# Kernel optimization log

Measured on AMD Instinct MI355X. Metric: run time of the kernel, lower is better.

## Reference

```python
import jax, jax.numpy as jnp
import numpy as np

NEG = -1.0e9  # masked_fill value from the original module

def setup_inputs() -> dict:
    key = jax.random.key(0)
    kq, kk, kv, km = jax.random.split(key, 4)
    B, H, S, D = 4, 16, 2048, 64
    Q = jax.random.normal(kq, (B, H, S, D), dtype=jnp.float32)
    K = jax.random.normal(kk, (B, H, S, D), dtype=jnp.float32)
    V = jax.random.normal(kv, (B, H, S, D), dtype=jnp.float32)
    # boolean mask, True = masked out (broadcast over batch and heads)
    mask = jax.random.randint(km, (1, 1, S, S), 0, 2).astype(jnp.bool_)
    return {"Q": Q, "K": K, "V": V, "mask": mask}

def reference(Q, K, V, mask):
    d_k = K.shape[-1]
    scale = 1.0 / jnp.sqrt(jnp.asarray(d_k, dtype=Q.dtype))
    # [B,H,S,S] attention scores
    scores = jnp.einsum("bhqd,bhkd->bhqk", Q, K) * scale
    scores = jnp.where(mask, jnp.asarray(NEG, dtype=scores.dtype), scores)
    weights = jax.nn.softmax(scores, axis=-1)
    # dropout is identity in eval mode (self.training == False)
    return jnp.einsum("bhqk,bhkd->bhqd", weights, V)
```

## Files before the change

### kernel.cpp

```cpp
#include <hip/hip_runtime.h>
#include <stdint.h>

#define SQ 2048
#define DH 64
#define NTILES (SQ / 64)

typedef __attribute__((ext_vector_type(8))) short bf16x8;
typedef __attribute__((ext_vector_type(4))) short bf16x4;
typedef __attribute__((ext_vector_type(4))) float f32x4;

static __device__ __forceinline__ unsigned short f2bf_rne(float x) {
  union { float f; uint32_t u; } v; v.f = x;
  uint32_t u = v.u;
  return (unsigned short)((u + 0x7FFFu + ((u >> 16) & 1u)) >> 16);
}

static __device__ __forceinline__ uint32_t pack_hi(float a, float b) {
  uint32_t au = __float_as_uint(a), bu = __float_as_uint(b);
#if __has_builtin(__builtin_amdgcn_perm)
  return __builtin_amdgcn_perm(bu, au, 0x07060302u);
#else
  return (bu & 0xFFFF0000u) | (au >> 16);
#endif
}

static __device__ __forceinline__ float fast_exp2(float x) {
#if __has_builtin(__builtin_amdgcn_exp2f)
  return __builtin_amdgcn_exp2f(x);
#else
  return exp2f(x);
#endif
}

#if __has_builtin(__builtin_amdgcn_mfma_f32_16x16x16_bf16)
#define MFMA_PV(a, b, c) __builtin_amdgcn_mfma_f32_16x16x16_bf16((a), (b), (c), 0, 0, 0)
#else
#define MFMA_PV(a, b, c) __builtin_amdgcn_mfma_f32_16x16x16bf16_1k((a), (b), (c), 0, 0, 0)
#endif

__global__ void pack_mask_kernel(const int* __restrict__ mask,
                                 unsigned long long* __restrict__ bits) {
  const int lane = threadIdx.x & 63;
  const int gw = (blockIdx.x * blockDim.x + threadIdx.x) >> 6;
  const int nw = (gridDim.x * blockDim.x) >> 6;
  for (int w = gw; w < SQ * SQ / 64; w += nw) {
    int v = mask[(size_t)w * 64 + lane];
    unsigned long long b = __ballot(v != 0);
    if (lane == 0) bits[(size_t)(w & 31) * SQ + (w >> 5)] = b;
  }
}

__global__ __launch_bounds__(512, 4) void attn_kernel(
    const float* __restrict__ Qg, const float* __restrict__ Kg,
    const float* __restrict__ Vg, const unsigned long long* __restrict__ mbits,
    const int* __restrict__ mraw, float* __restrict__ Og) {
  __shared__ __align__(16) unsigned short Klds[2][64][72];
  __shared__ __align__(16) uint32_t Vtlds[2][64][36];

  const int id = blockIdx.x;
  const int bh = id & 63;
  const int qblk = id >> 6;
  const int t = threadIdx.x;
  const int wave = t >> 6;
  const int lane = t & 63;
  const int col = lane & 15;
  const int quad = lane >> 4;

  const float* Qb = Qg + (size_t)bh * SQ * DH;
  const float* Kb = Kg + (size_t)bh * SQ * DH;
  const float* Vb = Vg + (size_t)bh * SQ * DH;
  float* Ob = Og + (size_t)bh * SQ * DH;

  const int q0 = qblk * 256 + wave * 32;

  const int skk = t >> 3;
  const int sd8 = (t & 7) * 8;
  const int skp = t >> 4;
  const int sd4 = (t & 15) * 4;

  const float QSCALE = 0.18033688011112042f;
  bf16x8 qf[2][2];
#pragma unroll
  for (int s = 0; s < 2; ++s) {
    int q = q0 + s * 16 + col;
#pragma unroll
    for (int j = 0; j < 2; ++j) {
      const float4* p = (const float4*)(Qb + (size_t)q * DH + j * 32 + quad * 8);
      float4 a = p[0], b = p[1];
      bf16x8 f;
      f[0] = (short)f2bf_rne(a.x * QSCALE); f[1] = (short)f2bf_rne(a.y * QSCALE);
      f[2] = (short)f2bf_rne(a.z * QSCALE); f[3] = (short)f2bf_rne(a.w * QSCALE);
      f[4] = (short)f2bf_rne(b.x * QSCALE); f[5] = (short)f2bf_rne(b.y * QSCALE);
      f[6] = (short)f2bf_rne(b.z * QSCALE); f[7] = (short)f2bf_rne(b.w * QSCALE);
      qf[s][j] = f;
    }
  }

  f32x4 acc[2][4];
  f32x4 accl[2];
#pragma unroll
  for (int s = 0; s < 2; ++s) {
#pragma unroll
    for (int dt = 0; dt < 4; ++dt)
#pragma unroll
      for (int r = 0; r < 4; ++r) acc[s][dt][r] = 0.0f;
#pragma unroll
    for (int r = 0; r < 4; ++r) accl[s][r] = 0.0f;
  }
  bf16x4 vones;
  vones[0] = (short)0x3F80; vones[1] = (short)0x3F80;
  vones[2] = (short)0x3F80; vones[3] = (short)0x3F80;
  const f32x4 fz = {0.0f, 0.0f, 0.0f, 0.0f};

  auto load_mask = [&](int ti, unsigned long long m[2]) {
    if (mbits) {
#pragma unroll
      for (int s = 0; s < 2; ++s)
        m[s] = mbits[(size_t)ti * SQ + (q0 + s * 16 + col)];
    } else {
#pragma unroll
      for (int s = 0; s < 2; ++s) {
        int q = q0 + s * 16 + col;
        unsigned long long mm = 0;
#pragma unroll
        for (int j = 0; j < 4; ++j) {
          int4 mi = *(const int4*)(mraw + (size_t)q * SQ + ti * 64 + j * 16 + quad * 4);
          unsigned long long nib = (unsigned long long)((mi.x != 0) | ((mi.y != 0) << 1) |
                                                        ((mi.z != 0) << 2) | ((mi.w != 0) << 3));
          mm |= nib << (j * 16 + quad * 4);
        }
        m[s] = mm;
      }
    }
  };

  {
    const float4* kp = (const float4*)(Kb + (size_t)skk * DH + sd8);
    float4 k0 = kp[0], k1 = kp[1];
    const float* va = Vb + (size_t)(skp * 2) * DH + sd4;
    float4 v0 = *(const float4*)va, v1 = *(const float4*)(va + DH);
    uint4 kw;
    kw.x = pack_hi(k0.x, k0.y); kw.y = pack_hi(k0.z, k0.w);
    kw.z = pack_hi(k1.x, k1.y); kw.w = pack_hi(k1.z, k1.w);
    *(uint4*)&Klds[0][skk][sd8] = kw;
    Vtlds[0][sd4 + 0][skp] = pack_hi(v0.x, v1.x);
    Vtlds[0][sd4 + 1][skp] = pack_hi(v0.y, v1.y);
    Vtlds[0][sd4 + 2][skp] = pack_hi(v0.z, v1.z);
    Vtlds[0][sd4 + 3][skp] = pack_hi(v0.w, v1.w);
  }
  unsigned long long mcur[2];
  load_mask(0, mcur);

  for (int tile = 0; tile < NTILES; ++tile) {
    __syncthreads();
    const int cb = tile & 1, nb = cb ^ 1;
    const int tn = (tile + 1 < NTILES) ? tile + 1 : tile;

    const int kkn = tn * 64;
    const float4* kp = (const float4*)(Kb + (size_t)(kkn + skk) * DH + sd8);
    float4 k0 = kp[0], k1 = kp[1];
    const float* va = Vb + (size_t)(kkn + skp * 2) * DH + sd4;
    float4 v0 = *(const float4*)va;
    float4 v1 = *(const float4*)(va + DH);
    unsigned long long mnxt[2];
    load_mask(tn, mnxt);

    uint32_t pfw[2][4][2];
#pragma unroll
    for (int kt = 0; kt < 4; ++kt) {
      const bf16x8 kf0 = *(const bf16x8*)&Klds[cb][kt * 16 + col][quad * 8];
      const bf16x8 kf1 = *(const bf16x8*)&Klds[cb][kt * 16 + col][32 + quad * 8];
#pragma unroll
      for (int s = 0; s < 2; ++s) {
        f32x4 st = __builtin_amdgcn_mfma_f32_16x16x32_bf16(kf0, qf[s][0], fz, 0, 0, 0);
        st = __builtin_amdgcn_mfma_f32_16x16x32_bf16(kf1, qf[s][1], st, 0, 0, 0);
        uint32_t nib = (uint32_t)(mcur[s] >> (kt * 16 + quad * 4)) & 0xFu;
        float p[4];
#pragma unroll
        for (int r = 0; r < 4; ++r)
          p[r] = fast_exp2(((nib >> r) & 1u) ? -1.0e9f : st[r]);
        pfw[s][kt][0] = pack_hi(p[0], p[1]);
        pfw[s][kt][1] = pack_hi(p[2], p[3]);
      }
    }

    {
      uint4 kw;
      kw.x = pack_hi(k0.x, k0.y); kw.y = pack_hi(k0.z, k0.w);
      kw.z = pack_hi(k1.x, k1.y); kw.w = pack_hi(k1.z, k1.w);
      *(uint4*)&Klds[nb][skk][sd8] = kw;
      Vtlds[nb][sd4 + 0][skp] = pack_hi(v0.x, v1.x);
      Vtlds[nb][sd4 + 1][skp] = pack_hi(v0.y, v1.y);
      Vtlds[nb][sd4 + 2][skp] = pack_hi(v0.z, v1.z);
      Vtlds[nb][sd4 + 3][skp] = pack_hi(v0.w, v1.w);
    }
    mcur[0] = mnxt[0]; mcur[1] = mnxt[1];

#pragma unroll
    for (int kt = 0; kt < 4; ++kt) {
      union { uint32_t u[2]; bf16x4 v; } p0, p1;
      p0.u[0] = pfw[0][kt][0]; p0.u[1] = pfw[0][kt][1];
      p1.u[0] = pfw[1][kt][0]; p1.u[1] = pfw[1][kt][1];
      accl[0] = MFMA_PV(vones, p0.v, accl[0]);
      accl[1] = MFMA_PV(vones, p1.v, accl[1]);
#pragma unroll
      for (int dt = 0; dt < 4; ++dt) {
        union { uint2 u2; bf16x4 v; } cv;
        cv.u2 = *(const uint2*)&Vtlds[cb][dt * 16 + col][kt * 8 + quad * 2];
        acc[0][dt] = MFMA_PV(cv.v, p0.v, acc[0][dt]);
        acc[1][dt] = MFMA_PV(cv.v, p1.v, acc[1][dt]);
      }
    }
  }

#pragma unroll
  for (int s = 0; s < 2; ++s) {
    float inv = 1.0f / accl[s][0];
    int q = q0 + s * 16 + col;
    float* orow = Ob + (size_t)q * DH;
#pragma unroll
    for (int dt = 0; dt < 4; ++dt) {
      float4 o;
      o.x = acc[s][dt][0] * inv;
      o.y = acc[s][dt][1] * inv;
      o.z = acc[s][dt][2] * inv;
      o.w = acc[s][dt][3] * inv;
      *(float4*)(orow + dt * 16 + quad * 4) = o;
    }
  }
}

extern "C" void kernel_launch(void* const* d_in, const int* in_sizes, int n_in,
                              void* d_out, int out_size, void* d_ws, size_t ws_size,
                              hipStream_t stream) {
  const float* Q = (const float*)d_in[0];
  const float* K = (const float*)d_in[1];
  const float* V = (const float*)d_in[2];
  const int* mask = (const int*)d_in[3];
  float* out = (float*)d_out;

  unsigned long long* bits = nullptr;
  const size_t need = (size_t)SQ * SQ / 8;
  if (ws_size >= need) {
    bits = (unsigned long long*)d_ws;
    pack_mask_kernel<<<1024, 256, 0, stream>>>(mask, bits);
  }
  attn_kernel<<<512, 512, 0, stream>>>(Q, K, V, bits, mask, out);
}
```

Before: 249.6 us.

## Pre-pack K/V to swizzled bf16 and mask to lane bitmasks before attention

New measurement: 242.8 us. 1.03x faster.

```diff
diff --git a/kernel.cpp b/kernel.cpp
--- a/kernel.cpp
+++ b/kernel.cpp
@@ -3,7 +3,6 @@
 
 #define SQ 2048
 #define DH 64
-#define NTILES (SQ / 64)
 
 typedef __attribute__((ext_vector_type(8))) short bf16x8;
 typedef __attribute__((ext_vector_type(4))) short bf16x4;
@@ -37,6 +36,77 @@
 #else
 #define MFMA_PV(a, b, c) __builtin_amdgcn_mfma_f32_16x16x16bf16_1k((a), (b), (c), 0, 0, 0)
 #endif
+
+
+__global__ __launch_bounds__(256) void pack_KV(const float* __restrict__ K,
+                                               const float* __restrict__ V,
+                                               uint4* __restrict__ pk,
+                                               uint2* __restrict__ pv) {
+  __shared__ uint32_t Vw[64][33];
+  const int bt = blockIdx.x;
+  const int t = threadIdx.x;
+  {
+    const float* src = K + (size_t)bt * 64 * DH;
+    uint4* dst = pk + (size_t)bt * 512;
+#pragma unroll
+    for (int j = 0; j < 2; ++j) {
+      int i = t + j * 256;
+      int kk = i >> 3, cp = i & 7;
+      int c = cp ^ (kk & 7);
+      const float4* s4 = (const float4*)(src + (size_t)kk * DH + c * 8);
+      float4 a = s4[0], b = s4[1];
+      uint4 w;
+      w.x = pack_hi(a.x, a.y); w.y = pack_hi(a.z, a.w);
+      w.z = pack_hi(b.x, b.y); w.w = pack_hi(b.z, b.w);
+      dst[i] = w;
+    }
+  }
+  {
+    const float* src = V + (size_t)bt * 64 * DH;
+#pragma unroll
+    for (int half = 0; half < 2; ++half) {
+      int kp = (t >> 4) + half * 16;
+      int d4 = (t & 15) * 4;
+      float4 a = *(const float4*)(src + (size_t)(2 * kp) * DH + d4);
+      float4 b = *(const float4*)(src + (size_t)(2 * kp + 1) * DH + d4);
+      Vw[d4 + 0][kp] = pack_hi(a.x, b.x);
+      Vw[d4 + 1][kp] = pack_hi(a.y, b.y);
+      Vw[d4 + 2][kp] = pack_hi(a.z, b.z);
+      Vw[d4 + 3][kp] = pack_hi(a.w, b.w);
+    }
+    __syncthreads();
+    uint2* dst = pv + (size_t)bt * 1024;
+#pragma unroll
+    for (int j = 0; j < 4; ++j) {
+      int o = t + j * 256;
+      int d = o >> 4, up = o & 15;
+      int u = up ^ (d & 15);
+      uint2 w;
+      w.x = Vw[d][2 * u]; w.y = Vw[d][2 * u + 1];
+      dst[o] = w;
+    }
+  }
+}
+
+__global__ __launch_bounds__(256) void pack_M(const int* __restrict__ mask,
+                                              uint2* __restrict__ pm) {
+  __shared__ uint2 Lm[16][17];
+  const int qb = blockIdx.x >> 5, gb = blockIdx.x & 31;
+  const int t = threadIdx.x;
+  {
+    int qq = t >> 4, gg = t & 15;
+    int4 m = *(const int4*)(mask + (size_t)(qb * 16 + qq) * SQ + (gb * 16 + gg) * 4);
+    uint2 w;
+    w.x = (m.x ? 0u : 0xFFFFu) | (m.y ? 0u : 0xFFFF0000u);
+    w.y = (m.z ? 0u : 0xFFFFu) | (m.w ? 0u : 0xFFFF0000u);
+    Lm[gg][qq] = w;
+  }
+  __syncthreads();
+  {
+    int gg = t >> 4, qq = t & 15;
+    pm[(size_t)(gb * 16 + gg) * 2048 + qb * 16 + qq] = Lm[gg][qq];
+  }
+}
 
 __global__ void pack_mask_kernel(const int* __restrict__ mask,
                                  unsigned long long* __restrict__ bits) {
@@ -50,33 +120,23 @@
   }
 }
 
-__global__ __launch_bounds__(512, 4) void attn_kernel(
-    const float* __restrict__ Qg, const float* __restrict__ Kg,
-    const float* __restrict__ Vg, const unsigned long long* __restrict__ mbits,
-    const int* __restrict__ mraw, float* __restrict__ Og) {
-  __shared__ __align__(16) unsigned short Klds[2][64][72];
-  __shared__ __align__(16) uint32_t Vtlds[2][64][36];
+__global__ __launch_bounds__(256, 4) void attn2(
+    const uint4* __restrict__ pk, const uint4* __restrict__ pv,
+    const uint2* __restrict__ pm, const float* __restrict__ Qg,
+    float* __restrict__ Og) {
+  __shared__ __align__(16) uint8_t smem[32768];
 
   const int id = blockIdx.x;
   const int bh = id & 63;
   const int qblk = id >> 6;
   const int t = threadIdx.x;
-  const int wave = t >> 6;
-  const int lane = t & 63;
-  const int col = lane & 15;
-  const int quad = lane >> 4;
+  const int wave = t >> 6, lane = t & 63, col = lane & 15, quad = lane >> 4;
 
   const float* Qb = Qg + (size_t)bh * SQ * DH;
-  const float* Kb = Kg + (size_t)bh * SQ * DH;
-  const float* Vb = Vg + (size_t)bh * SQ * DH;
   float* Ob = Og + (size_t)bh * SQ * DH;
-
-  const int q0 = qblk * 256 + wave * 32;
-
-  const int skk = t >> 3;
-  const int sd8 = (t & 7) * 8;
-  const int skp = t >> 4;
-  const int sd4 = (t & 15) * 4;
+  const uint4* pkb = pk + (size_t)bh * 32 * 512;
+  const uint4* pvb = pv + (size_t)bh * 32 * 512;
+  const int q0 = qblk * 128 + wave * 32;
 
   const float QSCALE = 0.18033688011112042f;
   bf16x8 qf[2][2];
@@ -96,6 +156,16 @@
     }
   }
 
+  const unsigned ka0 = col * 128 + ((quad ^ (col & 7)) * 16);
+  const unsigned ka1 = col * 128 + (((4 + quad) ^ (col & 7)) * 16);
+  unsigned va[4];
+#pragma unroll
+  for (int kt = 0; kt < 4; ++kt)
+    va[kt] = 16384u + col * 128 + (((kt * 4 + quad) ^ col) * 8);
+  const unsigned stK = t * 16;
+  const unsigned stV = 16384u + t * 16;
+  const size_t mqB = (size_t)(quad * 2048 + q0 + col) * 8;
+
   f32x4 acc[2][4];
   f32x4 accl[2];
 #pragma unroll
@@ -112,6 +182,134 @@
   vones[2] = (short)0x3F80; vones[3] = (short)0x3F80;
   const f32x4 fz = {0.0f, 0.0f, 0.0f, 0.0f};
 
+  {
+    uint4 k0 = pkb[t], k1 = pkb[t + 256];
+    uint4 v0 = pvb[t], v1 = pvb[t + 256];
+    *(uint4*)(smem + stK) = k0; *(uint4*)(smem + stK + 4096) = k1;
+    *(uint4*)(smem + stV) = v0; *(uint4*)(smem + stV + 4096) = v1;
+  }
+  unsigned buf = 0;
+
+  for (int tile = 0; tile < 32; ++tile) {
+    __syncthreads();
+    const int tn = (tile < 31) ? tile + 1 : 31;
+
+    const uint4* pkt = pkb + (size_t)tn * 512;
+    const uint4* pvt = pvb + (size_t)tn * 512;
+    uint4 k0 = pkt[t], k1 = pkt[t + 256];
+    uint4 v0 = pvt[t], v1 = pvt[t + 256];
+
+    const char* pmt = (const char*)pm + (size_t)tile * 262144 + mqB;
+    uint2 mw[2][4];
+#pragma unroll
+    for (int s = 0; s < 2; ++s)
+#pragma unroll
+      for (int kt = 0; kt < 4; ++kt)
+        mw[s][kt] = *(const uint2*)(pmt + (size_t)kt * 65536 + s * 128);
+
+    uint32_t pfw[2][4][2];
+#pragma unroll
+    for (int kt = 0; kt < 4; ++kt) {
+      const bf16x8 kf0 = *(const bf16x8*)(smem + buf + ka0 + kt * 2048);
+      const bf16x8 kf1 = *(const bf16x8*)(smem + buf + ka1 + kt * 2048);
+#pragma unroll
+      for (int s = 0; s < 2; ++s) {
+        f32x4 st = __builtin_amdgcn_mfma_f32_16x16x32_bf16(kf0, qf[s][0], fz, 0, 0, 0);
+        st = __builtin_amdgcn_mfma_f32_16x16x32_bf16(kf1, qf[s][1], st, 0, 0, 0);
+        float p0 = fast_exp2(st[0]), p1 = fast_exp2(st[1]);
+        float p2 = fast_exp2(st[2]), p3 = fast_exp2(st[3]);
+        pfw[s][kt][0] = pack_hi(p0, p1) & mw[s][kt].x;
+        pfw[s][kt][1] = pack_hi(p2, p3) & mw[s][kt].y;
+      }
+    }
+
+#pragma unroll
+    for (int kt = 0; kt < 4; ++kt) {
+      union { uint32_t u[2]; bf16x4 v; } p0, p1;
+      p0.u[0] = pfw[0][kt][0]; p0.u[1] = pfw[0][kt][1];
+      p1.u[0] = pfw[1][kt][0]; p1.u[1] = pfw[1][kt][1];
+      accl[0] = MFMA_PV(vones, p0.v, accl[0]);
+      accl[1] = MFMA_PV(vones, p1.v, accl[1]);
+#pragma unroll
+      for (int dt = 0; dt < 4; ++dt) {
+        union { uint2 u2; bf16x4 v; } cv;
+        cv.u2 = *(const uint2*)(smem + buf + va[kt] + dt * 2048);
+        acc[0][dt] = MFMA_PV(cv.v, p0.v, acc[0][dt]);
+        acc[1][dt] = MFMA_PV(cv.v, p1.v, acc[1][dt]);
+      }
+    }
+
+    const unsigned ob = buf ^ 8192u;
+    *(uint4*)(smem + ob + stK) = k0; *(uint4*)(smem + ob + stK + 4096) = k1;
+    *(uint4*)(smem + ob + stV) = v0; *(uint4*)(smem + ob + stV + 4096) = v1;
+    buf = ob;
+  }
+
+#pragma unroll
+  for (int s = 0; s < 2; ++s) {
+    float inv = 1.0f / accl[s][0];
+    int q = q0 + s * 16 + col;
+    float* orow = Ob + (size_t)q * DH;
+#pragma unroll
+    for (int dt = 0; dt < 4; ++dt) {
+      float4 o;
+      o.x = acc[s][dt][0] * inv;
+      o.y = acc[s][dt][1] * inv;
+      o.z = acc[s][dt][2] * inv;
+      o.w = acc[s][dt][3] * inv;
+      *(float4*)(orow + dt * 16 + quad * 4) = o;
+    }
+  }
+}
+
+__global__ __launch_bounds__(512, 4) void attn_fb(
+    const float* __restrict__ Qg, const float* __restrict__ Kg,
+    const float* __restrict__ Vg, const unsigned long long* __restrict__ mbits,
+    const int* __restrict__ mraw, float* __restrict__ Og) {
+  __shared__ __align__(16) unsigned short Klds[2][64][72];
+  __shared__ __align__(16) uint32_t Vtlds[2][64][36];
+  const int id = blockIdx.x;
+  const int bh = id & 63;
+  const int qblk = id >> 6;
+  const int t = threadIdx.x;
+  const int wave = t >> 6, lane = t & 63, col = lane & 15, quad = lane >> 4;
+  const float* Qb = Qg + (size_t)bh * SQ * DH;
+  const float* Kb = Kg + (size_t)bh * SQ * DH;
+  const float* Vb = Vg + (size_t)bh * SQ * DH;
+  float* Ob = Og + (size_t)bh * SQ * DH;
+  const int q0 = qblk * 256 + wave * 32;
+  const int skk = t >> 3, sd8 = (t & 7) * 8, skp = t >> 4, sd4 = (t & 15) * 4;
+  const float QSCALE = 0.18033688011112042f;
+  bf16x8 qf[2][2];
+#pragma unroll
+  for (int s = 0; s < 2; ++s) {
+    int q = q0 + s * 16 + col;
+#pragma unroll
+    for (int j = 0; j < 2; ++j) {
+      const float4* p = (const float4*)(Qb + (size_t)q * DH + j * 32 + quad * 8);
+      float4 a = p[0], b = p[1];
+      bf16x8 f;
+      f[0] = (short)f2bf_rne(a.x * QSCALE); f[1] = (short)f2bf_rne(a.y * QSCALE);
+      f[2] = (short)f2bf_rne(a.z * QSCALE); f[3] = (short)f2bf_rne(a.w * QSCALE);
+      f[4] = (short)f2bf_rne(b.x * QSCALE); f[5] = (short)f2bf_rne(b.y * QSCALE);
+      f[6] = (short)f2bf_rne(b.z * QSCALE); f[7] = (short)f2bf_rne(b.w * QSCALE);
+      qf[s][j] = f;
+    }
+  }
+  f32x4 acc[2][4]; f32x4 accl[2];
+#pragma unroll
+  for (int s = 0; s < 2; ++s) {
+#pragma unroll
+    for (int dt = 0; dt < 4; ++dt)
+#pragma unroll
+      for (int r = 0; r < 4; ++r) acc[s][dt][r] = 0.0f;
+#pragma unroll
+    for (int r = 0; r < 4; ++r) accl[s][r] = 0.0f;
+  }
+  bf16x4 vones;
+  vones[0] = (short)0x3F80; vones[1] = (short)0x3F80;
+  vones[2] = (short)0x3F80; vones[3] = (short)0x3F80;
+  const f32x4 fz = {0.0f, 0.0f, 0.0f, 0.0f};
   auto load_mask = [&](int ti, unsigned long long m[2]) {
     if (mbits) {
 #pragma unroll
@@ -133,7 +331,6 @@
       }
     }
   };
-
   {
     const float4* kp = (const float4*)(Kb + (size_t)skk * DH + sd8);
     float4 k0 = kp[0], k1 = kp[1];
@@ -150,12 +347,10 @@
   }
   unsigned long long mcur[2];
   load_mask(0, mcur);
-
-  for (int tile = 0; tile < NTILES; ++tile) {
+  for (int tile = 0; tile < 32; ++tile) {
     __syncthreads();
     const int cb = tile & 1, nb = cb ^ 1;
-    const int tn = (tile + 1 < NTILES) ? tile + 1 : tile;
-
+    const int tn = (tile + 1 < 32) ? tile + 1 : tile;
     const int kkn = tn * 64;
     const float4* kp = (const float4*)(Kb + (size_t)(kkn + skk) * DH + sd8);
     float4 k0 = kp[0], k1 = kp[1];
@@ -164,7 +359,6 @@
     float4 v1 = *(const float4*)(va + DH);
     unsigned long long mnxt[2];
     load_mask(tn, mnxt);
-
     uint32_t pfw[2][4][2];
 #pragma unroll
     for (int kt = 0; kt < 4; ++kt) {
@@ -183,7 +377,6 @@
         pfw[s][kt][1] = pack_hi(p[2], p[3]);
       }
     }
-
     {
       uint4 kw;
       kw.x = pack_hi(k0.x, k0.y); kw.y = pack_hi(k0.z, k0.w);
@@ -195,7 +388,6 @@
       Vtlds[nb][sd4 + 3][skp] = pack_hi(v0.w, v1.w);
     }
     mcur[0] = mnxt[0]; mcur[1] = mnxt[1];
-
 #pragma unroll
     for (int kt = 0; kt < 4; ++kt) {
       union { uint32_t u[2]; bf16x4 v; } p0, p1;
@@ -212,7 +404,6 @@
       }
     }
   }
-
 #pragma unroll
   for (int s = 0; s < 2; ++s) {
     float inv = 1.0f / accl[s][0];
@@ -239,11 +430,23 @@
   const int* mask = (const int*)d_in[3];
   float* out = (float*)d_out;
 
-  unsigned long long* bits = nullptr;
-  const size_t need = (size_t)SQ * SQ / 8;
-  if (ws_size >= need) {
-    bits = (unsigned long long*)d_ws;
+  const size_t PK_BYTES = (size_t)64 * 32 * 8192;
+  const size_t PV_BYTES = (size_t)64 * 32 * 8192;
+  const size_t PM_BYTES = (size_t)512 * 2048 * 8;
+  const size_t NEED = PK_BYTES + PV_BYTES + PM_BYTES;
+
+  if (ws_size >= NEED) {
+    uint4* pk = (uint4*)d_ws;
+    uint2* pv = (uint2*)((char*)d_ws + PK_BYTES);
+    uint2* pm = (uint2*)((char*)d_ws + PK_BYTES + PV_BYTES);
+    pack_KV<<<2048, 256, 0, stream>>>(K, V, pk, (uint2*)pv);
+    pack_M<<<4096, 256, 0, stream>>>(mask, pm);
+    attn2<<<1024, 256, 0, stream>>>(pk, (uint4*)pv, pm, Q, out);
+  } else if (ws_size >= (size_t)SQ * SQ / 8) {
+    unsigned long long* bits = (unsigned long long*)d_ws;
     pack_mask_kernel<<<1024, 256, 0, stream>>>(mask, bits);
-  }
-  attn_kernel<<<512, 512, 0, stream>>>(Q, K, V, bits, mask, out);
-}
+    attn_fb<<<512, 512, 0, stream>>>(Q, K, V, bits, mask, out);
+  } else {
+    attn_fb<<<512, 512, 0, stream>>>(Q, K, V, nullptr, mask, out);
+  }
+}
```
